# Performance work log

Measured on AMD Instinct MI355X. Metric: run time of the kernel, lower is better.

Reference implementation:

```python
import jax, jax.numpy as jnp
import numpy as np

ALPHA = 0.5

def setup_inputs() -> dict:
    key = jax.random.key(0)
    k1, k2 = jax.random.split(key)
    B, S, F_IN, F_OUT = 64, 512, 1024, 1024
    x = jax.random.normal(k1, (B, S, F_IN), dtype=jnp.float32)
    W = jax.random.normal(k2, (F_OUT, F_IN), dtype=jnp.float32) * (F_IN ** -0.5)
    return {"x": x, "W": W}

def reference(x, W):
    # x: [B, S, F_in], W: [F_out, F_in] (torch Linear layout, no bias)
    alpha = jnp.asarray(ALPHA, dtype=x.dtype)
    # Project all segments at once (the big GEMM), then scan the EMA recurrence.
    y = jnp.einsum('bsf,of->bso', x, W)  # [B, S, F_out]
    y_t = jnp.swapaxes(y, 0, 1)          # [S, B, F_out] for scan over segments

    def step(h, yk):
        h = alpha * h + (1 - alpha) * yk
        return h, h

    h0 = jnp.zeros((x.shape[0], W.shape[0]), dtype=x.dtype)
    hk, hiddens_t = jax.lax.scan(step, h0, y_t)
    hiddens = jnp.swapaxes(hiddens_t, 0, 1)  # [B, S, F_out]
    return (hk, hiddens)
```

## Files before the change

kernel.cpp:

```cpp
#include <hip/hip_runtime.h>
#include <hip/hip_bf16.h>
#include <stdint.h>

#define B_DIM 64
#define S_DIM 512
#define K_DIM 1024
#define N_DIM 1024
#define M_DIM (B_DIM * S_DIM)

typedef __attribute__((ext_vector_type(8))) short short8;
typedef __attribute__((ext_vector_type(4))) float floatx4;

__global__ __launch_bounds__(256) void scan_x_kernel(
    const float* __restrict__ x, __hip_bfloat16* __restrict__ xs) {
  const int t  = blockIdx.x * 256 + threadIdx.x;
  const int f4 = (t & 255) << 2;
  const int c  = (t >> 8) & 7;
  const int b  = t >> 11;
  const size_t base = (size_t)b * S_DIM * K_DIM + f4;
  const int s0 = c * 64;

  float4 h = {0.f, 0.f, 0.f, 0.f};
  if (c != 0) {
    #pragma unroll 8
    for (int s = s0 - 32; s < s0; ++s) {
      float4 v = *(const float4*)(x + base + (size_t)s * K_DIM);
      h.x = 0.5f * (h.x + v.x); h.y = 0.5f * (h.y + v.y);
      h.z = 0.5f * (h.z + v.z); h.w = 0.5f * (h.w + v.w);
    }
  }
  #pragma unroll 8
  for (int s = s0; s < s0 + 64; ++s) {
    float4 v = *(const float4*)(x + base + (size_t)s * K_DIM);
    h.x = 0.5f * (h.x + v.x); h.y = 0.5f * (h.y + v.y);
    h.z = 0.5f * (h.z + v.z); h.w = 0.5f * (h.w + v.w);
    __hip_bfloat16 b0 = __float2bfloat16(h.x);
    __hip_bfloat16 b1 = __float2bfloat16(h.y);
    __hip_bfloat16 b2 = __float2bfloat16(h.z);
    __hip_bfloat16 b3 = __float2bfloat16(h.w);
    union { unsigned short u[4]; uint2 v2; } pk;
    pk.u[0] = *(unsigned short*)&b0; pk.u[1] = *(unsigned short*)&b1;
    pk.u[2] = *(unsigned short*)&b2; pk.u[3] = *(unsigned short*)&b3;
    *(uint2*)(xs + base + (size_t)s * K_DIM) = pk.v2;
  }
}

__global__ __launch_bounds__(256) void conv_w_kernel(
    const float* __restrict__ W, __hip_bfloat16* __restrict__ Wb) {
  int t = blockIdx.x * 256 + threadIdx.x;
  Wb[t] = __float2bfloat16(W[t]);
}

__global__ __launch_bounds__(256) void gemm_kernel(
    const __hip_bfloat16* __restrict__ A,
    const __hip_bfloat16* __restrict__ Bw,
    float* __restrict__ out) {
  __shared__ __hip_bfloat16 lA[128 * 32];
  __shared__ __hip_bfloat16 lB[128 * 32];

  const int tid  = threadIdx.x;
  const int lane = tid & 63;
  const int w    = tid >> 6;
  const int wm   = (w >> 1) * 64;
  const int wn   = (w & 1) * 64;
  const int quad = lane >> 4;
  const int l15  = lane & 15;
  const int sw   = ((quad ^ ((l15 >> 1) & 3)) * 8);

  const int n0 = blockIdx.x * 128;
  const int m0 = blockIdx.y * 128;

  floatx4 acc[4][4] = {};

  for (int k0 = 0; k0 < K_DIM; k0 += 32) {
    #pragma unroll
    for (int p = 0; p < 2; ++p) {
      int c    = tid + p * 256;
      int r    = c >> 2;
      int slot = c & 3;
      int kc   = (slot ^ ((r >> 1) & 3)) * 8;
      const __hip_bfloat16* ga = A  + (size_t)(m0 + r) * K_DIM + k0 + kc;
      const __hip_bfloat16* gb = Bw + (size_t)(n0 + r) * K_DIM + k0 + kc;
      __builtin_amdgcn_global_load_lds(
          (const __attribute__((address_space(1))) void*)ga,
          (__attribute__((address_space(3))) void*)&lA[c * 8], 16, 0, 0);
      __builtin_amdgcn_global_load_lds(
          (const __attribute__((address_space(1))) void*)gb,
          (__attribute__((address_space(3))) void*)&lB[c * 8], 16, 0, 0);
    }
    __syncthreads();

    short8 af[4], bfr[4];
    #pragma unroll
    for (int i = 0; i < 4; ++i) {
      af[i]  = *(const short8*)&lA[(wm + i * 16 + l15) * 32 + sw];
      bfr[i] = *(const short8*)&lB[(wn + i * 16 + l15) * 32 + sw];
    }
    #pragma unroll
    for (int i = 0; i < 4; ++i)
      #pragma unroll
      for (int j = 0; j < 4; ++j)
        acc[i][j] = __builtin_amdgcn_mfma_f32_16x16x32_bf16(
            af[i], bfr[j], acc[i][j], 0, 0, 0);
    __syncthreads();
  }

  float* hid = out + B_DIM * N_DIM;
  #pragma unroll
  for (int i = 0; i < 4; ++i) {
    #pragma unroll
    for (int j = 0; j < 4; ++j) {
      #pragma unroll
      for (int r = 0; r < 4; ++r) {
        int gm = m0 + wm + i * 16 + quad * 4 + r;
        int gn = n0 + wn + j * 16 + l15;
        float v = acc[i][j][r];
        hid[(size_t)gm * N_DIM + gn] = v;
        if ((gm & (S_DIM - 1)) == (S_DIM - 1)) {
          out[(size_t)(gm >> 9) * N_DIM + gn] = v;
        }
      }
    }
  }
}

extern "C" void kernel_launch(void* const* d_in, const int* in_sizes, int n_in,
                              void* d_out, int out_size, void* d_ws, size_t ws_size,
                              hipStream_t stream) {
  const float* x = (const float*)d_in[0];
  const float* W = (const float*)d_in[1];
  float* out = (float*)d_out;

  __hip_bfloat16* xs = (__hip_bfloat16*)d_ws;
  __hip_bfloat16* Wb = (__hip_bfloat16*)((char*)d_ws + (size_t)M_DIM * K_DIM * 2);

  scan_x_kernel<<<dim3(131072 / 256), dim3(256), 0, stream>>>(x, xs);
  conv_w_kernel<<<dim3((N_DIM * K_DIM) / 256), dim3(256), 0, stream>>>(W, Wb);
  gemm_kernel<<<dim3(N_DIM / 128, M_DIM / 128), dim3(256), 0, stream>>>(xs, Wb, out);
}
```

Measured before the change: 343.9 us.

## Double-buffer GEMM LDS tiles, remap blocks per XCD, vectorize epilogue stores

The GEMM now double-buffers its LDS tiles, issuing the next K-tile's global-to-LDS loads right after the barrier so they overlap the MFMAs, and drops the second barrier per iteration. LDS is reorganized into a k-chunk-major layout in place of the XOR swizzle. Operands are swapped in the MFMA so each lane holds four consecutive output columns, allowing float4 stores in the epilogue. Blocks are launched as a 1D grid remapped so each XCD gets a contiguous group of M-tiles for L2 reuse. Separately, the scan warm-up window shrinks from 32 to 16 steps, which cuts reads but raises the truncation error to 2^-16, still at bf16 precision.

```diff
diff --git a/kernel.cpp b/kernel.cpp
--- a/kernel.cpp
+++ b/kernel.cpp
@@ -7,6 +7,8 @@
 #define K_DIM 1024
 #define N_DIM 1024
 #define M_DIM (B_DIM * S_DIM)
+#define BK 32
+#define KTILES (K_DIM / BK)
 
 typedef __attribute__((ext_vector_type(8))) short short8;
 typedef __attribute__((ext_vector_type(4))) float floatx4;
@@ -23,7 +25,7 @@
   float4 h = {0.f, 0.f, 0.f, 0.f};
   if (c != 0) {
     #pragma unroll 8
-    for (int s = s0 - 32; s < s0; ++s) {
+    for (int s = s0 - 16; s < s0; ++s) {
       float4 v = *(const float4*)(x + base + (size_t)s * K_DIM);
       h.x = 0.5f * (h.x + v.x); h.y = 0.5f * (h.y + v.y);
       h.z = 0.5f * (h.z + v.z); h.w = 0.5f * (h.w + v.w);
@@ -51,12 +53,12 @@
   Wb[t] = __float2bfloat16(W[t]);
 }
 
-__global__ __launch_bounds__(256) void gemm_kernel(
+__global__ __launch_bounds__(256, 4) void gemm_kernel(
     const __hip_bfloat16* __restrict__ A,
     const __hip_bfloat16* __restrict__ Bw,
     float* __restrict__ out) {
-  __shared__ __hip_bfloat16 lA[128 * 32];
-  __shared__ __hip_bfloat16 lB[128 * 32];
+  __shared__ __hip_bfloat16 lA[2][128 * BK];
+  __shared__ __hip_bfloat16 lB[2][128 * BK];
 
   const int tid  = threadIdx.x;
   const int lane = tid & 63;
@@ -65,61 +67,66 @@
   const int wn   = (w & 1) * 64;
   const int quad = lane >> 4;
   const int l15  = lane & 15;
-  const int sw   = ((quad ^ ((l15 >> 1) & 3)) * 8);
 
-  const int n0 = blockIdx.x * 128;
-  const int m0 = blockIdx.y * 128;
+  const int bi    = blockIdx.x;
+  const int xcd   = bi & 7;
+  const int local = bi >> 3;
+  const int m0 = (xcd * 32 + (local >> 3)) * 128;
+  const int n0 = (local & 7) * 128;
+
+  auto stage = [&](int t, int bsel) {
+    const int k0 = t * BK;
+    #pragma unroll
+    for (int p = 0; p < 2; ++p) {
+      int c = tid + p * 256;
+      int q = c >> 7;
+      int r = c & 127;
+      const __hip_bfloat16* ga = A  + (size_t)(m0 + r) * K_DIM + k0 + q * 8;
+      const __hip_bfloat16* gb = Bw + (size_t)(n0 + r) * K_DIM + k0 + q * 8;
+      __builtin_amdgcn_global_load_lds(
+          (const __attribute__((address_space(1))) void*)ga,
+          (__attribute__((address_space(3))) void*)&lA[bsel][c * 8], 16, 0, 0);
+      __builtin_amdgcn_global_load_lds(
+          (const __attribute__((address_space(1))) void*)gb,
+          (__attribute__((address_space(3))) void*)&lB[bsel][c * 8], 16, 0, 0);
+    }
+  };
 
   floatx4 acc[4][4] = {};
+  stage(0, 0);
 
-  for (int k0 = 0; k0 < K_DIM; k0 += 32) {
-    #pragma unroll
-    for (int p = 0; p < 2; ++p) {
-      int c    = tid + p * 256;
-      int r    = c >> 2;
-      int slot = c & 3;
-      int kc   = (slot ^ ((r >> 1) & 3)) * 8;
-      const __hip_bfloat16* ga = A  + (size_t)(m0 + r) * K_DIM + k0 + kc;
-      const __hip_bfloat16* gb = Bw + (size_t)(n0 + r) * K_DIM + k0 + kc;
-      __builtin_amdgcn_global_load_lds(
-          (const __attribute__((address_space(1))) void*)ga,
-          (__attribute__((address_space(3))) void*)&lA[c * 8], 16, 0, 0);
-      __builtin_amdgcn_global_load_lds(
-          (const __attribute__((address_space(1))) void*)gb,
-          (__attribute__((address_space(3))) void*)&lB[c * 8], 16, 0, 0);
-    }
+  for (int t = 0; t < KTILES; ++t) {
     __syncthreads();
+    if (t + 1 < KTILES) stage(t + 1, (t + 1) & 1);
 
+    const __hip_bfloat16* bufA = lA[t & 1];
+    const __hip_bfloat16* bufB = lB[t & 1];
     short8 af[4], bfr[4];
     #pragma unroll
-    for (int i = 0; i < 4; ++i) {
-      af[i]  = *(const short8*)&lA[(wm + i * 16 + l15) * 32 + sw];
-      bfr[i] = *(const short8*)&lB[(wn + i * 16 + l15) * 32 + sw];
-    }
+    for (int i = 0; i < 4; ++i)
+      af[i]  = *(const short8*)&bufA[(quad * 128 + wm + i * 16 + l15) * 8];
+    #pragma unroll
+    for (int j = 0; j < 4; ++j)
+      bfr[j] = *(const short8*)&bufB[(quad * 128 + wn + j * 16 + l15) * 8];
     #pragma unroll
     for (int i = 0; i < 4; ++i)
       #pragma unroll
       for (int j = 0; j < 4; ++j)
         acc[i][j] = __builtin_amdgcn_mfma_f32_16x16x32_bf16(
-            af[i], bfr[j], acc[i][j], 0, 0, 0);
-    __syncthreads();
+            bfr[j], af[i], acc[i][j], 0, 0, 0);
   }
 
   float* hid = out + B_DIM * N_DIM;
   #pragma unroll
   for (int i = 0; i < 4; ++i) {
+    const int gm = m0 + wm + i * 16 + l15;
+    const bool is_last = (gm & (S_DIM - 1)) == (S_DIM - 1);
     #pragma unroll
     for (int j = 0; j < 4; ++j) {
-      #pragma unroll
-      for (int r = 0; r < 4; ++r) {
-        int gm = m0 + wm + i * 16 + quad * 4 + r;
-        int gn = n0 + wn + j * 16 + l15;
-        float v = acc[i][j][r];
-        hid[(size_t)gm * N_DIM + gn] = v;
-        if ((gm & (S_DIM - 1)) == (S_DIM - 1)) {
-          out[(size_t)(gm >> 9) * N_DIM + gn] = v;
-        }
-      }
+      const int gn = n0 + wn + j * 16 + quad * 4;
+      *(floatx4*)&hid[(size_t)gm * N_DIM + gn] = acc[i][j];
+      if (is_last)
+        *(floatx4*)&out[(size_t)(gm >> 9) * N_DIM + gn] = acc[i][j];
     }
   }
 }
@@ -136,5 +143,5 @@
 
   scan_x_kernel<<<dim3(131072 / 256), dim3(256), 0, stream>>>(x, xs);
   conv_w_kernel<<<dim3((N_DIM * K_DIM) / 256), dim3(256), 0, stream>>>(W, Wb);
-  gemm_kernel<<<dim3(N_DIM / 128, M_DIM / 128), dim3(256), 0, stream>>>(xs, Wb, out);
+  gemm_kernel<<<dim3((M_DIM / 128) * (N_DIM / 128)), dim3(256), 0, stream>>>(xs, Wb, out);
 }
```

New measurement: 375.9 us. 9.3% more time.
